# Optimization experiments

Measured on AMD Instinct MI355X. Metric: run time of the kernel, lower is better.

Reference implementation:

```python
import jax, jax.numpy as jnp
import numpy as np

N = 100000      # op nodes
E = 1600000     # feed edges
C = 8           # num_configs
H = 64          # hidden_dim
OPE = 64        # op_embed_dim
NF = 140        # per-node dense features
CF = 18         # per-config features
NUM_OPS = 120
B = 16          # graphs per batch (context segments)
IN_DIM = OPE + NF + CF  # 222
ALPHA = 0.2     # tf.nn.leaky_relu default slope


def setup_inputs() -> dict:
    key = jax.random.key(0)
    ks = jax.random.split(key, 32)

    def w(k, shape, fan_in):
        return jax.random.normal(k, shape, jnp.float32) * (1.0 / np.sqrt(fan_in))

    inp = {
        'node_feats': jax.random.normal(ks[0], (N, NF), jnp.float32),
        'config_feats': jax.random.normal(ks[1], (N, C, CF), jnp.float32),
        'op_ids': jax.random.randint(ks[2], (N,), 0, NUM_OPS, jnp.int32),
        'src': jax.random.randint(ks[3], (E,), 0, N, jnp.int32),
        'dst': jax.random.randint(ks[4], (E,), 0, N, jnp.int32),
        'graph_ids': jnp.sort(jax.random.randint(ks[5], (N,), 0, B, jnp.int32)),
        'op_emb': jax.random.normal(ks[6], (NUM_OPS, OPE), jnp.float32) * 0.05,
        # GNN layer 0 (input dim 222), layers 1,2 (dim 64)
        'W_d0': w(ks[7], (IN_DIM, H), IN_DIM), 'b_d0': jnp.zeros((H,), jnp.float32),
        'W_p0': w(ks[8], (IN_DIM, H), IN_DIM), 'b_p0': jnp.zeros((H,), jnp.float32),
        'W_d1': w(ks[9], (H, H), H), 'b_d1': jnp.zeros((H,), jnp.float32),
        'W_p1': w(ks[10], (H, H), H), 'b_p1': jnp.zeros((H,), jnp.float32),
        'W_d2': w(ks[11], (H, H), H), 'b_d2': jnp.zeros((H,), jnp.float32),
        'W_p2': w(ks[12], (H, H), H), 'b_p2': jnp.zeros((H,), jnp.float32),
        # postnet MLP: Dense(64) -> act -> Dense(64) -> act -> Dense(1)
        'W_m0': w(ks[13], (H, H), H), 'b_m0': jnp.zeros((H,), jnp.float32),
        'W_m1': w(ks[14], (H, H), H), 'b_m1': jnp.zeros((H,), jnp.float32),
        'W_m2': w(ks[15], (H, 1), H), 'b_m2': jnp.zeros((1,), jnp.float32),
    }
    return inp


def _leaky(x):
    return jax.nn.leaky_relu(x, negative_slope=ALPHA)


def _l2norm(x):  # tf.nn.l2_normalize(axis=-1), eps=1e-12
    sq = jnp.sum(x * x, axis=-1, keepdims=True)
    return x * jax.lax.rsqrt(jnp.maximum(sq, 1e-12))


def reference(node_feats, config_feats, op_ids, src, dst, graph_ids, op_emb,
              W_d0, b_d0, W_p0, b_p0, W_d1, b_d1, W_p1, b_p1,
              W_d2, b_d2, W_p2, b_p2, W_m0, b_m0, W_m1, b_m1, W_m2, b_m2):
    # early-join op embedding + node feats (broadcast over configs) + config feats
    base = jnp.concatenate([op_emb[op_ids], node_feats], axis=-1)  # [N, OPE+NF]
    x = jnp.concatenate(
        [jnp.broadcast_to(base[:, None, :], (N, C, OPE + NF)), config_feats],
        axis=-1)  # [N, C, 222]

    def adj_mul(v):  # bidirectional feed adjacency: A + A^T
        return (jax.ops.segment_sum(v[src], dst, num_segments=N)
                + jax.ops.segment_sum(v[dst], src, num_segments=N))

    for (Wd, bd, Wp, bp) in ((W_d0, b_d0, W_p0, b_p0),
                             (W_d1, b_d1, W_p1, b_p1),
                             (W_d2, b_d2, W_p2, b_p2)):
        y = adj_mul(x)                                  # [N, C, D] spmm
        y = _leaky(jnp.einsum('ncd,dh->nch', y, Wd) + bd)
        x = jnp.einsum('ncd,dh->nch', x, Wp) + bp + y   # residual
        x = _l2norm(x)

    pooled = jax.ops.segment_sum(x, graph_ids, num_segments=B)  # [B, C, H]

    h = _leaky(jnp.einsum('bch,hk->bck', pooled, W_m0) + b_m0)
    h = _leaky(jnp.einsum('bch,hk->bck', h, W_m1) + b_m1)
    out = jnp.einsum('bch,hk->bck', h, W_m2) + b_m2     # [B, C, 1]
    return jnp.squeeze(out, -1)                         # [B, C]
```

## Files before the change

### kernel.cpp

```cpp
#include <hip/hip_runtime.h>
#include <hip/hip_bf16.h>

#define NN 100000
#define EE 1600000
#define CC 8
#define HH 64
#define NF 140
#define CF 18
#define BB 16
#define NROWS (NN * CC)
#define ALPHA 0.2f


typedef unsigned short u16;
typedef unsigned int u32;
typedef unsigned char u8;
typedef __attribute__((ext_vector_type(8))) short short8;
typedef __attribute__((ext_vector_type(4))) float f32x4;
typedef __attribute__((ext_vector_type(4))) float fv4;
typedef __attribute__((ext_vector_type(2))) float f32x2;

__device__ __forceinline__ float rdlane(float v, int l) {
    return __int_as_float(__builtin_amdgcn_readlane(__float_as_int(v), l));
}
__device__ __forceinline__ float lrelu(float x) { return x > 0.f ? x : ALPHA * x; }
__device__ __forceinline__ float wave_sum64(float v) {
#pragma unroll
    for (int m = 1; m < 64; m <<= 1) v += __shfl_xor(v, m, 64);
    return v;
}
__device__ __forceinline__ float b2f(u16 u) { return __uint_as_float(((u32)u) << 16); }
__device__ __forceinline__ u32 f2b(float f) {
    u32 u = __float_as_uint(f);
    return (u + 0x7fffu + ((u >> 16) & 1u)) >> 16;
}
__device__ __forceinline__ u32 pack2(float lo, float hi) {
    return f2b(lo) | (f2b(hi) << 16);
}
__device__ __forceinline__ short8 ld_frag(const u16* p) {
    union { uint4 u; short8 s; } c;
    c.u = *(const uint4*)p;
    return c.s;
}

#if __has_builtin(__builtin_amdgcn_cvt_pk_f32_fp8) && __has_builtin(__builtin_amdgcn_cvt_pk_fp8_f32)
#define HAS_HW_FP8 1
#else
#define HAS_HW_FP8 0
#endif

__device__ __forceinline__ float dec8_sw(u32 b) {
    u32 u = ((b & 0x80u) << 24) | ((b & 0x7fu) << 20);
    return __uint_as_float(u) * 0x1.0p+120f;
}
__device__ __forceinline__ u32 enc8_sw(float f) {
    f = fminf(fmaxf(f, -448.f), 448.f);
    u32 u = __float_as_uint(f * 0x1.0p-120f);
    u32 r = u + 0x7ffffu + ((u >> 20) & 1u);
    return ((r >> 24) & 0x80u) | ((r >> 20) & 0x7fu);
}
__device__ __forceinline__ u32 pk4_fp8(float a, float b, float c, float d) {
#if HAS_HW_FP8
    u32 w = 0;
    w = __builtin_amdgcn_cvt_pk_fp8_f32(a, b, w, false);
    w = __builtin_amdgcn_cvt_pk_fp8_f32(c, d, w, true);
    return w;
#else
    return enc8_sw(a) | (enc8_sw(b) << 8) | (enc8_sw(c) << 16) | (enc8_sw(d) << 24);
#endif
}
__device__ __forceinline__ void accf8(float* a, uint2 t) {
#if HAS_HW_FP8
    f32x2 d;
    d = __builtin_amdgcn_cvt_pk_f32_fp8(t.x, false); a[0] += d.x; a[1] += d.y;
    d = __builtin_amdgcn_cvt_pk_f32_fp8(t.x, true);  a[2] += d.x; a[3] += d.y;
    d = __builtin_amdgcn_cvt_pk_f32_fp8(t.y, false); a[4] += d.x; a[5] += d.y;
    d = __builtin_amdgcn_cvt_pk_f32_fp8(t.y, true);  a[6] += d.x; a[7] += d.y;
#else
    u32 w[2] = {t.x, t.y};
#pragma unroll
    for (int q = 0; q < 2; q++) {
        a[q*4+0] += dec8_sw(w[q] & 0xffu);
        a[q*4+1] += dec8_sw((w[q] >> 8) & 0xffu);
        a[q*4+2] += dec8_sw((w[q] >> 16) & 0xffu);
        a[q*4+3] += dec8_sw((w[q] >> 24) & 0xffu);
    }
#endif
}

__global__ __launch_bounds__(256) void deg_count_k(const int* __restrict__ src,
                                                   const int* __restrict__ dst,
                                                   int* __restrict__ deg) {
    int e = blockIdx.x * 256 + threadIdx.x;
    if (e < EE) atomicAdd(&deg[dst[e]], 1);
    else if (e < 2 * EE) atomicAdd(&deg[src[e - EE]], 1);
}

__global__ __launch_bounds__(1024) void scan1_k(const int* __restrict__ deg,
                                                int* __restrict__ row_ptr,
                                                int* __restrict__ bsum, int n) {
    __shared__ int lds[17];
    int i = blockIdx.x * 1024 + threadIdx.x;
    int lane = threadIdx.x & 63, wv = threadIdx.x >> 6;
    int val = (i < n) ? deg[i] : 0;
    int v = val;
#pragma unroll
    for (int d = 1; d < 64; d <<= 1) {
        int t = __shfl_up(v, d, 64);
        if (lane >= d) v += t;
    }
    if (lane == 63) lds[wv] = v;
    __syncthreads();
    if (threadIdx.x == 0) {
        int run = 0;
#pragma unroll
        for (int k = 0; k < 16; k++) { int t = lds[k]; lds[k] = run; run += t; }
        lds[16] = run;
    }
    __syncthreads();
    if (i < n) row_ptr[i] = v - val + lds[wv];
    if (threadIdx.x == 1023) bsum[blockIdx.x] = lds[16];
}

__global__ void scan2_k(int* __restrict__ bsum, int nb) {
    int run = 0;
    for (int b = 0; b < nb; b++) { int t = bsum[b]; bsum[b] = run; run += t; }
    bsum[nb] = run;
}

__global__ __launch_bounds__(1024) void scan3_k(int* __restrict__ row_ptr,
                                                int* __restrict__ cursor,
                                                const int* __restrict__ bsum,
                                                int n, int nb) {
    int i = blockIdx.x * 1024 + threadIdx.x;
    if (i < n) {
        int v = row_ptr[i] + bsum[blockIdx.x];
        row_ptr[i] = v;
        cursor[i] = v;
    }
    if (i == 0) row_ptr[n] = bsum[nb];
}

__global__ __launch_bounds__(256) void place_k(const int* __restrict__ src,
                                               const int* __restrict__ dst,
                                               int* __restrict__ cursor,
                                               int* __restrict__ col,
                                               int c0, int c1) {
    int e = blockIdx.x * 256 + threadIdx.x;
    int node, other;
    if (e < EE) { node = dst[e]; other = src[e]; }
    else if (e < 2 * EE) { node = src[e - EE]; other = dst[e - EE]; }
    else return;
    if (node < c0 || node >= c1) return;
    int pos = atomicAdd(&cursor[node], 1);
    col[pos] = other;
}

__global__ __launch_bounds__(256) void prep_w_k(const float* __restrict__ Wd1, const float* __restrict__ Wp1,
                                                const float* __restrict__ Wd2, const float* __restrict__ Wp2,
                                                const float* __restrict__ Wd0nf, const float* __restrict__ Wp0nf,
                                                u16* __restrict__ WT) {
    int i = blockIdx.x * 256 + threadIdx.x;
    if (i < 4 * 4096) {
        int w = i >> 12, idx = i & 4095;
        int n = idx >> 6, k = idx & 63;
        const float* W = (w == 0) ? Wd1 : (w == 1) ? Wp1 : (w == 2) ? Wd2 : Wp2;
        WT[w * 4096 + n * 64 + k] = (u16)f2b(W[k * 64 + n]);
    } else {
        int j = i - 4 * 4096;
        if (j < 2 * 64 * 160) {
            int w = j / 10240, idx = j % 10240;
            int n = idx / 160, k = idx % 160;
            const float* W = w ? Wp0nf : Wd0nf;
            WT[16384 + w * 10240 + n * 160 + k] = (k < 140) ? (u16)f2b(W[k * 64 + n]) : (u16)0;
        }
    }
}

__global__ __launch_bounds__(256) void op_dp_k(const float* __restrict__ op_emb,
                                               const float* __restrict__ Wd_top,
                                               const float* __restrict__ Wp_top,
                                               float* __restrict__ op_d,
                                               float* __restrict__ op_p) {
    int lane = threadIdx.x & 63;
    int wid = (blockIdx.x * 256 + threadIdx.x) >> 6;
    if (wid >= 120) return;
    float v = op_emb[wid * 64 + lane];
    float ad = 0.f, ap = 0.f;
    for (int k = 0; k < 64; k++) {
        float s = rdlane(v, k);
        ad = fmaf(s, Wd_top[k * 64 + lane], ad);
        ap = fmaf(s, Wp_top[k * 64 + lane], ap);
    }
    op_d[wid * 64 + lane] = ad;
    op_p[wid * 64 + lane] = ap;
}

__global__ __launch_bounds__(256) void nf_mfma_k(const float* __restrict__ nf,
                                                 const u16* __restrict__ WdT0,
                                                 const u16* __restrict__ WpT0,
                                                 u16* __restrict__ nf_d,
                                                 u16* __restrict__ nf_p) {
    int lane = threadIdx.x & 63;
    int m = lane & 15, q = lane >> 4;
    int wid = (blockIdx.x * 256 + threadIdx.x) >> 6;
    int nw = (gridDim.x * 256) >> 6;
    for (int rb = wid; rb < NN / 16; rb += nw) {
        int node0 = rb * 16;
        const float* row = nf + (size_t)(node0 + m) * 140;
        short8 af[5];
#pragma unroll
        for (int s = 0; s < 5; s++) {
            int k0 = s * 32 + q * 8;
            float f[8];
            if (s < 4) {
                fv4 lo = __builtin_nontemporal_load((const fv4*)(row + k0));
                fv4 hi = __builtin_nontemporal_load((const fv4*)(row + k0 + 4));
                f[0]=lo.x; f[1]=lo.y; f[2]=lo.z; f[3]=lo.w;
                f[4]=hi.x; f[5]=hi.y; f[6]=hi.z; f[7]=hi.w;
            } else {
#pragma unroll
                for (int j = 0; j < 8; j++) f[j] = 0.f;
                if (q == 0) {
                    fv4 lo = __builtin_nontemporal_load((const fv4*)(row + 128));
                    fv4 hi = __builtin_nontemporal_load((const fv4*)(row + 132));
                    f[0]=lo.x; f[1]=lo.y; f[2]=lo.z; f[3]=lo.w;
                    f[4]=hi.x; f[5]=hi.y; f[6]=hi.z; f[7]=hi.w;
                } else if (q == 1) {
                    fv4 lo = __builtin_nontemporal_load((const fv4*)(row + 136));
                    f[0]=lo.x; f[1]=lo.y; f[2]=lo.z; f[3]=lo.w;
                }
            }
            short8 t;
#pragma unroll
            for (int j = 0; j < 8; j++) t[j] = (short)f2b(f[j]);
            af[s] = t;
        }
        f32x4 ad[4], ap[4];
#pragma unroll
        for (int t = 0; t < 4; t++) {
            ad[t] = (f32x4){0.f, 0.f, 0.f, 0.f};
            ap[t] = (f32x4){0.f, 0.f, 0.f, 0.f};
        }
#pragma unroll
        for (int s = 0; s < 5; s++) {
#pragma unroll
            for (int t = 0; t < 4; t++) {
                int boff = (t * 16 + m) * 160 + s * 32 + q * 8;
                short8 bdw = ld_frag(WdT0 + boff);
                short8 bpw = ld_frag(WpT0 + boff);
                ad[t] = __builtin_amdgcn_mfma_f32_16x16x32_bf16(af[s], bdw, ad[t], 0, 0, 0);
                ap[t] = __builtin_amdgcn_mfma_f32_16x16x32_bf16(af[s], bpw, ap[t], 0, 0, 0);
            }
        }
#pragma unroll
        for (int r = 0; r < 4; r++) {
            size_t nrow = (size_t)(node0 + q * 4 + r);
#pragma unroll
            for (int t = 0; t < 4; t++) {
                nf_d[nrow * 64 + t * 16 + m] = (u16)f2b(ad[t][r]);
                nf_p[nrow * 64 + t * 16 + m] = (u16)f2b(ap[t][r]);
            }
        }
    }
}

__global__ __launch_bounds__(256) void hd0_dual_k(u8* __restrict__ G,
                                                  u16* __restrict__ Y,
                                                  const float* __restrict__ cf,
                                                  const int* __restrict__ op_ids,
                                                  const u16* __restrict__ nf_d,
                                                  const u16* __restrict__ nf_p,
                                                  const float* __restrict__ op_d,
                                                  const float* __restrict__ op_p,
                                                  const float* __restrict__ WdBot,
                                                  const float* __restrict__ WpBot) {
    int lane = threadIdx.x & 63;
    float wbd[18], wbp[18];
#pragma unroll
    for (int k = 0; k < 18; k++) { wbd[k] = WdBot[k * 64 + lane]; wbp[k] = WpBot[k * 64 + lane]; }
    int wid = (blockIdx.x * 256 + threadIdx.x) >> 6;
    int nw = (gridDim.x * 256) >> 6;
    for (int row = wid; row < NROWS; row += nw) {
        int n = row >> 3;
        float cfv = (lane < 18) ? __builtin_nontemporal_load(cf + (size_t)row * 18 + lane) : 0.f;
        int op = op_ids[n];
        float accd = op_d[op * 64 + lane] + b2f(nf_d[(size_t)n * 64 + lane]);
        float accp = op_p[op * 64 + lane] + b2f(nf_p[(size_t)n * 64 + lane]);
#pragma unroll
        for (int k = 0; k < 18; k++) {
            float s = rdlane(cfv, k);
            accd = fmaf(s, wbd[k], accd);
            accp = fmaf(s, wbp[k], accp);
        }
        float f1 = __shfl_down(accd, 1, 64);
        float f2 = __shfl_down(accd, 2, 64);
        float f3 = __shfl_down(accd, 3, 64);
        if ((lane & 3) == 0)
            ((u32*)G)[(size_t)row * 16 + (lane >> 2)] = pk4_fp8(accd, f1, f2, f3);
        Y[(size_t)row * 64 + lane] = (u16)f2b(accp);
    }
}

__global__ __launch_bounds__(256) void conv_fp8_k(const u16* __restrict__ src,
                                                  uint2* __restrict__ dst) {
    int i = blockIdx.x * 256 + threadIdx.x;
    if (i >= NROWS * 64 / 8) return;
    short8 v = ld_frag(src + (size_t)i * 8);
    float f[8];
#pragma unroll
    for (int k = 0; k < 8; k++) f[k] = b2f((u16)v[k]);
    uint2 o;
    o.x = pk4_fp8(f[0], f[1], f[2], f[3]);
    o.y = pk4_fp8(f[4], f[5], f[6], f[7]);
    dst[i] = o;
}

__global__ __launch_bounds__(256) void fused_l0_f8_k(const u8* __restrict__ G,
                                                     u16* __restrict__ Y,
                                                     const int* __restrict__ row_ptr,
                                                     const int* __restrict__ col,
                                                     const float* __restrict__ bd,
                                                     const float* __restrict__ bp) {
    int wid = (blockIdx.x * 256 + threadIdx.x) >> 6;
    int lane = threadIdx.x & 63;
    if (wid >= NN) return;
    int r = lane >> 3, fb = (lane & 7) * 8;
    const uint2* G2 = (const uint2*)G;
    int start = row_ptr[wid];
    int end = row_ptr[wid + 1];
    float a[8] = {0.f, 0.f, 0.f, 0.f, 0.f, 0.f, 0.f, 0.f};
    int j = start;
    for (; j + 16 <= end; j += 16) {
        uint2 t[16];
#pragma unroll
        for (int u = 0; u < 16; u++) t[u] = G2[(size_t)col[j + u] * 64 + lane];
#pragma unroll
        for (int u = 0; u < 16; u++) accf8(a, t[u]);
    }
    for (; j + 4 <= end; j += 4) {
        uint2 t[4];
#pragma unroll
        for (int u = 0; u < 4; u++) t[u] = G2[(size_t)col[j + u] * 64 + lane];
#pragma unroll
        for (int u = 0; u < 4; u++) accf8(a, t[u]);
    }
    for (; j < end; j++) {
        uint2 t0 = G2[(size_t)col[j] * 64 + lane];
        accf8(a, t0);
    }
    float bdv[8], bpv[8];
#pragma unroll
    for (int jj = 0; jj < 8; jj++) { bdv[jj] = bd[fb + jj]; bpv[jj] = bp[fb + jj]; }
    size_t rowg = (size_t)wid * 8 + r;
    short8 xp = ld_frag(Y + rowg * 64 + fb);
    float v[8], sq = 0.f;
#pragma unroll
    for (int q = 0; q < 8; q++) {
        float val = b2f((u16)xp[q]) + bpv[q] + lrelu(a[q] + bdv[q]);
        v[q] = val;
        sq += val * val;
    }
    sq += __shfl_xor(sq, 1, 64);
    sq += __shfl_xor(sq, 2, 64);
    sq += __shfl_xor(sq, 4, 64);
    float sc = rsqrtf(fmaxf(sq, 1e-12f));
    uint4 o;
    o.x = pack2(v[0] * sc, v[1] * sc);
    o.y = pack2(v[2] * sc, v[3] * sc);
    o.z = pack2(v[4] * sc, v[5] * sc);
    o.w = pack2(v[6] * sc, v[7] * sc);
    *(uint4*)(Y + rowg * 64 + fb) = o;
}

__global__ __launch_bounds__(256) void fused_spmm_f8_k(u16* __restrict__ Y,
                                                       const u8* __restrict__ G,
                                                       const int* __restrict__ row_ptr,
                                                       const int* __restrict__ col,
                                                       const u16* __restrict__ WdT,
                                                       const u16* __restrict__ WpT,
                                                       const float* __restrict__ bd,
                                                       const float* __restrict__ bp) {
    __shared__ u16 lds_t[4 * 16 * 72];
    int lane = threadIdx.x & 63;
    u16* L = lds_t + (threadIdx.x >> 6) * (16 * 72);
    int m = lane & 15, q = lane >> 4;
    const uint2* G2 = (const uint2*)G;

    int wid = (blockIdx.x * 256 + threadIdx.x) >> 6;
    if (wid >= NN / 2) return;
    int pb = wid;

#pragma unroll
    for (int p = 0; p < 2; p++) {
        int node = pb * 2 + p;
        int start = row_ptr[node], end = row_ptr[node + 1];
        float a[8] = {0.f, 0.f, 0.f, 0.f, 0.f, 0.f, 0.f, 0.f};
        int j = start;
        for (; j + 16 <= end; j += 16) {
            uint2 t[16];
#pragma unroll
            for (int u = 0; u < 16; u++) t[u] = G2[(size_t)col[j + u] * 64 + lane];
#pragma unroll
            for (int u = 0; u < 16; u++) accf8(a, t[u]);
        }
        for (; j + 4 <= end; j += 4) {
            uint2 t[4];
#pragma unroll
            for (int u = 0; u < 4; u++) t[u] = G2[(size_t)col[j + u] * 64 + lane];
#pragma unroll
            for (int u = 0; u < 4; u++) accf8(a, t[u]);
        }
        for (; j < end; j++) {
            uint2 t0 = G2[(size_t)col[j] * 64 + lane];
            accf8(a, t0);
        }
        uint4 o;
        o.x = pack2(a[0], a[1]);
        o.y = pack2(a[2], a[3]);
        o.z = pack2(a[4], a[5]);
        o.w = pack2(a[6], a[7]);
        *(uint4*)(L + (size_t)(p * 8 + (lane >> 3)) * 72 + (lane & 7) * 8) = o;
    }
    __builtin_amdgcn_sched_barrier(0);

    short8 ay0 = ld_frag(L + m * 72 + q * 8);
    short8 ay1 = ld_frag(L + m * 72 + 32 + q * 8);
    const u16* xr = Y + ((size_t)(pb * 16 + m)) * 64 + q * 8;
    short8 ax0 = ld_frag(xr), ax1 = ld_frag(xr + 32);
    float v[4][4], sq[4];
#pragma unroll
    for (int r = 0; r < 4; r++) sq[r] = 0.f;
#pragma unroll 1
    for (int t = 0; t < 4; t++) {
        int off = (t * 16 + m) * 64 + q * 8;
        short8 bd0 = ld_frag(WdT + off), bd1 = ld_frag(WdT + off + 32);
        short8 bp0 = ld_frag(WpT + off), bp1 = ld_frag(WpT + off + 32);
        f32x4 ad = (f32x4){0.f, 0.f, 0.f, 0.f};
        f32x4 ap = (f32x4){0.f, 0.f, 0.f, 0.f};
        ad = __builtin_amdgcn_mfma_f32_16x16x32_bf16(ay0, bd0, ad, 0, 0, 0);
        ad = __builtin_amdgcn_mfma_f32_16x16x32_bf16(ay1, bd1, ad, 0, 0, 0);
        ap = __builtin_amdgcn_mfma_f32_16x16x32_bf16(ax0, bp0, ap, 0, 0, 0);
        ap = __builtin_amdgcn_mfma_f32_16x16x32_bf16(ax1, bp1, ap, 0, 0, 0);
        float bdv = bd[t * 16 + m], bpv = bp[t * 16 + m];
#pragma unroll
        for (int r = 0; r < 4; r++) {
            float val = ap[r] + bpv + lrelu(ad[r] + bdv);
            v[t][r] = val;
            sq[r] += val * val;
        }
    }
#pragma unroll
    for (int r = 0; r < 4; r++) {
#pragma unroll
        for (int mm = 1; mm < 16; mm <<= 1) sq[r] += __shfl_xor(sq[r], mm, 64);
        float sc = rsqrtf(fmaxf(sq[r], 1e-12f));
        u16* orow = Y + ((size_t)(pb * 16 + q * 4 + r)) * 64 + m;
#pragma unroll
        for (int t = 0; t < 4; t++) orow[t * 16] = (u16)f2b(v[t][r] * sc);
    }
}

__global__ __launch_bounds__(256) void pool2_k(const u16* __restrict__ X,
                                               const int* __restrict__ graph_ids,
                                               float* __restrict__ pooled) {
    int chunk = (NN + gridDim.x - 1) / gridDim.x;
    int n0 = blockIdx.x * chunk;
    int n1 = min(n0 + chunk, NN);
    if (n0 >= n1) return;
    int f = threadIdx.x & 63;
    int c0 = threadIdx.x >> 6;
    float a0 = 0.f, a1 = 0.f;
    int cur = graph_ids[n0];
    for (int n = n0; n < n1; n++) {
        int g = graph_ids[n];
        if (g != cur) {
            atomicAdd(&pooled[(size_t)(cur * 8 + c0) * 64 + f], a0);
            atomicAdd(&pooled[(size_t)(cur * 8 + c0 + 4) * 64 + f], a1);
            a0 = 0.f; a1 = 0.f; cur = g;
        }
        a0 += b2f(X[((size_t)n * 8 + c0) * 64 + f]);
        a1 += b2f(X[((size_t)n * 8 + c0 + 4) * 64 + f]);
    }
    atomicAdd(&pooled[(size_t)(cur * 8 + c0) * 64 + f], a0);
    atomicAdd(&pooled[(size_t)(cur * 8 + c0 + 4) * 64 + f], a1);
}

__global__ __launch_bounds__(256) void mlp_k(const float* __restrict__ pooled,
                                             const float* __restrict__ W0, const float* __restrict__ b0,
                                             const float* __restrict__ W1, const float* __restrict__ b1,
                                             const float* __restrict__ W2, const float* __restrict__ b2,
                                             float* __restrict__ out) {
    int lane = threadIdx.x & 63;
    int row = blockIdx.x * 4 + (threadIdx.x >> 6);
    if (row >= BB * CC) return;
    float b0l = b0[lane], b1l = b1[lane], w2l = W2[lane], b2s = b2[0];
    float p = pooled[(size_t)row * 64 + lane];
    float a = 0.f;
    for (int k = 0; k < 64; k++) a = fmaf(rdlane(p, k), W0[k * 64 + lane], a);
    float h0 = lrelu(a + b0l);
    float a1 = 0.f;
    for (int k = 0; k < 64; k++) a1 = fmaf(rdlane(h0, k), W1[k * 64 + lane], a1);
    float h1 = lrelu(a1 + b1l);
    float v = wave_sum64(h1 * w2l);
    if (lane == 0) out[row] = v + b2s;
}

extern "C" void kernel_launch(void* const* d_in, const int* in_sizes, int n_in,
                              void* d_out, int out_size, void* d_ws, size_t ws_size,
                              hipStream_t stream) {
    const float* node_feats   = (const float*)d_in[0];
    const float* config_feats = (const float*)d_in[1];
    const int*   op_ids       = (const int*)d_in[2];
    const int*   src          = (const int*)d_in[3];
    const int*   dst          = (const int*)d_in[4];
    const int*   graph_ids    = (const int*)d_in[5];
    const float* op_emb       = (const float*)d_in[6];
    const float* W_d0 = (const float*)d_in[7],  *b_d0 = (const float*)d_in[8];
    const float* W_p0 = (const float*)d_in[9],  *b_p0 = (const float*)d_in[10];
    const float* W_d1 = (const float*)d_in[11], *b_d1 = (const float*)d_in[12];
    const float* W_p1 = (const float*)d_in[13], *b_p1 = (const float*)d_in[14];
    const float* W_d2 = (const float*)d_in[15], *b_d2 = (const float*)d_in[16];
    const float* W_p2 = (const float*)d_in[17], *b_p2 = (const float*)d_in[18];
    const float* W_m0 = (const float*)d_in[19], *b_m0 = (const float*)d_in[20];
    const float* W_m1 = (const float*)d_in[21], *b_m1 = (const float*)d_in[22];
    const float* W_m2 = (const float*)d_in[23], *b_m2 = (const float*)d_in[24];
    float* out = (float*)d_out;

    char* ws = (char*)d_ws;
    size_t off = 0;
    u16* Y       = (u16*)(ws + off); off += (size_t)NROWS * 64 * 2;
    u8*  G       = (u8*)(ws + off);  off += (size_t)NROWS * 64;
    int* col     = (int*)(ws + off);   off += (size_t)2 * EE * 4;
    int* row_ptr = (int*)(ws + off);   off += 400128;
    u16* WT      = (u16*)(ws + off);   off += (4 * 4096 + 2 * 10240) * 2;
    float* pooled = (float*)(ws + off); off += BB * CC * 64 * 4;
    u16* nf_d    = (u16*)(ws + off); off += (size_t)NN * 64 * 2;
    u16* nf_p    = (u16*)(ws + off); off += (size_t)NN * 64 * 2;
    float* op_d  = (float*)(ws + off); off += 120 * 64 * 4;
    float* op_p  = (float*)(ws + off); off += 120 * 64 * 4;
    int* deg     = (int*)(ws + off);   off += 400128;
    int* cursor  = (int*)(ws + off);   off += 400128;
    int* bsum    = (int*)(ws + off);   off += 512;
    (void)ws_size; (void)in_sizes; (void)n_in; (void)out_size;

    const int NB = (NN + 1023) / 1024;
    const int NCONV = (NROWS * 64 / 8 + 255) / 256;

    hipMemsetAsync(deg, 0, (size_t)NN * 4, stream);
    hipMemsetAsync(pooled, 0, (size_t)BB * CC * 64 * 4, stream);
    deg_count_k<<<(2 * EE) / 256, 256, 0, stream>>>(src, dst, deg);
    prep_w_k<<<144, 256, 0, stream>>>(W_d1, W_p1, W_d2, W_p2,
                                      W_d0 + 64 * 64, W_p0 + 64 * 64, WT);
    scan1_k<<<NB, 1024, 0, stream>>>(deg, row_ptr, bsum, NN);
    scan2_k<<<1, 1, 0, stream>>>(bsum, NB);
    scan3_k<<<NB, 1024, 0, stream>>>(row_ptr, cursor, bsum, NN, NB);
    {
        const int NCHUNK = 8;
        const int CSZ = (NN + NCHUNK - 1) / NCHUNK;
        for (int c = 0; c < NCHUNK; c++) {
            int c0 = c * CSZ;
            int c1 = min(c0 + CSZ, NN);
            place_k<<<(2 * EE) / 256, 256, 0, stream>>>(src, dst, cursor, col, c0, c1);
        }
    }

    op_dp_k<<<30, 256, 0, stream>>>(op_emb, W_d0, W_p0, op_d, op_p);
    nf_mfma_k<<<512, 256, 0, stream>>>(node_feats, WT + 16384, WT + 16384 + 10240, nf_d, nf_p);
    hd0_dual_k<<<2048, 256, 0, stream>>>(G, Y, config_feats, op_ids, nf_d, nf_p,
                                         op_d, op_p, W_d0 + 204 * 64, W_p0 + 204 * 64);

    fused_l0_f8_k<<<NN / 4, 256, 0, stream>>>(G, Y, row_ptr, col, b_d0, b_p0);
    conv_fp8_k<<<NCONV, 256, 0, stream>>>(Y, (uint2*)G);
    fused_spmm_f8_k<<<12500, 256, 0, stream>>>(Y, G, row_ptr, col,
                                               WT, WT + 4096, b_d1, b_p1);
    conv_fp8_k<<<NCONV, 256, 0, stream>>>(Y, (uint2*)G);
    fused_spmm_f8_k<<<12500, 256, 0, stream>>>(Y, G, row_ptr, col,
                                               WT + 8192, WT + 12288, b_d2, b_p2);

    pool2_k<<<2048, 256, 0, stream>>>(Y, graph_ids, pooled);
    mlp_k<<<32, 256, 0, stream>>>(pooled, W_m0, b_m0, W_m1, b_m1, W_m2, b_m2, out);
}
```

Before: 1.536 ms.

## Merge setup kernels, parallelize block-sum scan, widen fp8 conversion, halve placement passes

Merges the degree count, weight prep and op-embedding projection into one launch that dispatches on block index. The serial single-thread block-sum scan becomes a 128-thread wave scan. The fp8 conversion kernel now handles 16 values per thread with 128-bit stores. Edge placement runs in 4 chunked passes instead of 8, which cuts launches but may add atomic contention per pass. Together these aim to reduce launch count and small serial overheads in the graph-setup phase.

```diff
diff --git a/kernel.cpp b/kernel.cpp
--- a/kernel.cpp
+++ b/kernel.cpp
@@ -88,12 +88,62 @@
 #endif
 }
 
-__global__ __launch_bounds__(256) void deg_count_k(const int* __restrict__ src,
-                                                   const int* __restrict__ dst,
-                                                   int* __restrict__ deg) {
-    int e = blockIdx.x * 256 + threadIdx.x;
-    if (e < EE) atomicAdd(&deg[dst[e]], 1);
-    else if (e < 2 * EE) atomicAdd(&deg[src[e - EE]], 1);
+#define SETUP_DEG_BLK 12500
+#define SETUP_PW_BLK  144
+#define SETUP_OP_BLK  30
+__global__ __launch_bounds__(256) void setup_k(const int* __restrict__ src,
+                                               const int* __restrict__ dst,
+                                               int* __restrict__ deg,
+                                               const float* __restrict__ Wd1, const float* __restrict__ Wp1,
+                                               const float* __restrict__ Wd2, const float* __restrict__ Wp2,
+                                               const float* __restrict__ Wd0nf, const float* __restrict__ Wp0nf,
+                                               u16* __restrict__ WT,
+                                               const float* __restrict__ op_emb,
+                                               const float* __restrict__ Wd_top,
+                                               const float* __restrict__ Wp_top,
+                                               float* __restrict__ op_d,
+                                               float* __restrict__ op_p) {
+    int b = blockIdx.x;
+    if (b < SETUP_DEG_BLK) {
+        int e = b * 256 + threadIdx.x;
+        if (e < EE) atomicAdd(&deg[dst[e]], 1);
+        else if (e < 2 * EE) atomicAdd(&deg[src[e - EE]], 1);
+        return;
+    }
+    b -= SETUP_DEG_BLK;
+    if (b < SETUP_PW_BLK) {
+        int i = b * 256 + threadIdx.x;
+        if (i < 4 * 4096) {
+            int w = i >> 12, idx = i & 4095;
+            int n = idx >> 6, k = idx & 63;
+            const float* W = (w == 0) ? Wd1 : (w == 1) ? Wp1 : (w == 2) ? Wd2 : Wp2;
+            WT[w * 4096 + n * 64 + k] = (u16)f2b(W[k * 64 + n]);
+        } else {
+            int j = i - 4 * 4096;
+            if (j < 2 * 64 * 160) {
+                int w = j / 10240, idx = j % 10240;
+                int n = idx / 160, k = idx % 160;
+                const float* W = w ? Wp0nf : Wd0nf;
+                WT[16384 + w * 10240 + n * 160 + k] = (k < 140) ? (u16)f2b(W[k * 64 + n]) : (u16)0;
+            }
+        }
+        return;
+    }
+    b -= SETUP_PW_BLK;
+    {
+        int lane = threadIdx.x & 63;
+        int wid = (b * 256 + threadIdx.x) >> 6;
+        if (wid >= 120) return;
+        float v = op_emb[wid * 64 + lane];
+        float ad = 0.f, ap = 0.f;
+        for (int k = 0; k < 64; k++) {
+            float s = rdlane(v, k);
+            ad = fmaf(s, Wd_top[k * 64 + lane], ad);
+            ap = fmaf(s, Wp_top[k * 64 + lane], ap);
+        }
+        op_d[wid * 64 + lane] = ad;
+        op_p[wid * 64 + lane] = ap;
+    }
 }
 
 __global__ __launch_bounds__(1024) void scan1_k(const int* __restrict__ deg,
@@ -122,10 +172,22 @@
     if (threadIdx.x == 1023) bsum[blockIdx.x] = lds[16];
 }
 
-__global__ void scan2_k(int* __restrict__ bsum, int nb) {
-    int run = 0;
-    for (int b = 0; b < nb; b++) { int t = bsum[b]; bsum[b] = run; run += t; }
-    bsum[nb] = run;
+__global__ __launch_bounds__(128) void scan2_k(int* __restrict__ bsum, int nb) {
+    __shared__ int wsum[2];
+    int tid = threadIdx.x;
+    int lane = tid & 63, wv = tid >> 6;
+    int val = (tid < nb) ? bsum[tid] : 0;
+    int v = val;
+#pragma unroll
+    for (int d = 1; d < 64; d <<= 1) {
+        int t = __shfl_up(v, d, 64);
+        if (lane >= d) v += t;
+    }
+    if (lane == 63) wsum[wv] = v;
+    __syncthreads();
+    int incl = v + ((wv == 1) ? wsum[0] : 0);
+    if (tid < nb) bsum[tid] = incl - val;
+    if (tid == 127) bsum[nb] = incl;
 }
 
 __global__ __launch_bounds__(1024) void scan3_k(int* __restrict__ row_ptr,
@@ -156,46 +218,6 @@
     col[pos] = other;
 }
 
-__global__ __launch_bounds__(256) void prep_w_k(const float* __restrict__ Wd1, const float* __restrict__ Wp1,
-                                                const float* __restrict__ Wd2, const float* __restrict__ Wp2,
-                                                const float* __restrict__ Wd0nf, const float* __restrict__ Wp0nf,
-                                                u16* __restrict__ WT) {
-    int i = blockIdx.x * 256 + threadIdx.x;
-    if (i < 4 * 4096) {
-        int w = i >> 12, idx = i & 4095;
-        int n = idx >> 6, k = idx & 63;
-        const float* W = (w == 0) ? Wd1 : (w == 1) ? Wp1 : (w == 2) ? Wd2 : Wp2;
-        WT[w * 4096 + n * 64 + k] = (u16)f2b(W[k * 64 + n]);
-    } else {
-        int j = i - 4 * 4096;
-        if (j < 2 * 64 * 160) {
-            int w = j / 10240, idx = j % 10240;
-            int n = idx / 160, k = idx % 160;
-            const float* W = w ? Wp0nf : Wd0nf;
-            WT[16384 + w * 10240 + n * 160 + k] = (k < 140) ? (u16)f2b(W[k * 64 + n]) : (u16)0;
-        }
-    }
-}
-
-__global__ __launch_bounds__(256) void op_dp_k(const float* __restrict__ op_emb,
-                                               const float* __restrict__ Wd_top,
-                                               const float* __restrict__ Wp_top,
-                                               float* __restrict__ op_d,
-                                               float* __restrict__ op_p) {
-    int lane = threadIdx.x & 63;
-    int wid = (blockIdx.x * 256 + threadIdx.x) >> 6;
-    if (wid >= 120) return;
-    float v = op_emb[wid * 64 + lane];
-    float ad = 0.f, ap = 0.f;
-    for (int k = 0; k < 64; k++) {
-        float s = rdlane(v, k);
-        ad = fmaf(s, Wd_top[k * 64 + lane], ad);
-        ap = fmaf(s, Wp_top[k * 64 + lane], ap);
-    }
-    op_d[wid * 64 + lane] = ad;
-    op_p[wid * 64 + lane] = ap;
-}
-
 __global__ __launch_bounds__(256) void nf_mfma_k(const float* __restrict__ nf,
                                                  const u16* __restrict__ WdT0,
                                                  const u16* __restrict__ WpT0,
@@ -303,16 +325,19 @@
 }
 
 __global__ __launch_bounds__(256) void conv_fp8_k(const u16* __restrict__ src,
-                                                  uint2* __restrict__ dst) {
+                                                  uint4* __restrict__ dst) {
     int i = blockIdx.x * 256 + threadIdx.x;
-    if (i >= NROWS * 64 / 8) return;
-    short8 v = ld_frag(src + (size_t)i * 8);
-    float f[8];
-#pragma unroll
-    for (int k = 0; k < 8; k++) f[k] = b2f((u16)v[k]);
-    uint2 o;
+    if (i >= NROWS * 4) return;
+    short8 v0 = ld_frag(src + (size_t)i * 16);
+    short8 v1 = ld_frag(src + (size_t)i * 16 + 8);
+    float f[16];
+#pragma unroll
+    for (int k = 0; k < 8; k++) { f[k] = b2f((u16)v0[k]); f[k + 8] = b2f((u16)v1[k]); }
+    uint4 o;
     o.x = pk4_fp8(f[0], f[1], f[2], f[3]);
     o.y = pk4_fp8(f[4], f[5], f[6], f[7]);
+    o.z = pk4_fp8(f[8], f[9], f[10], f[11]);
+    o.w = pk4_fp8(f[12], f[13], f[14], f[15]);
     dst[i] = o;
 }
 
@@ -545,18 +570,19 @@
     (void)ws_size; (void)in_sizes; (void)n_in; (void)out_size;
 
     const int NB = (NN + 1023) / 1024;
-    const int NCONV = (NROWS * 64 / 8 + 255) / 256;
+    const int NCONV = NROWS * 4 / 256;
 
     hipMemsetAsync(deg, 0, (size_t)NN * 4, stream);
     hipMemsetAsync(pooled, 0, (size_t)BB * CC * 64 * 4, stream);
-    deg_count_k<<<(2 * EE) / 256, 256, 0, stream>>>(src, dst, deg);
-    prep_w_k<<<144, 256, 0, stream>>>(W_d1, W_p1, W_d2, W_p2,
-                                      W_d0 + 64 * 64, W_p0 + 64 * 64, WT);
+    setup_k<<<SETUP_DEG_BLK + SETUP_PW_BLK + SETUP_OP_BLK, 256, 0, stream>>>(
+        src, dst, deg,
+        W_d1, W_p1, W_d2, W_p2, W_d0 + 64 * 64, W_p0 + 64 * 64, WT,
+        op_emb, W_d0, W_p0, op_d, op_p);
     scan1_k<<<NB, 1024, 0, stream>>>(deg, row_ptr, bsum, NN);
-    scan2_k<<<1, 1, 0, stream>>>(bsum, NB);
+    scan2_k<<<1, 128, 0, stream>>>(bsum, NB);
     scan3_k<<<NB, 1024, 0, stream>>>(row_ptr, cursor, bsum, NN, NB);
     {
-        const int NCHUNK = 8;
+        const int NCHUNK = 4;
         const int CSZ = (NN + NCHUNK - 1) / NCHUNK;
         for (int c = 0; c < NCHUNK; c++) {
             int c0 = c * CSZ;
@@ -565,16 +591,15 @@
         }
     }
 
-    op_dp_k<<<30, 256, 0, stream>>>(op_emb, W_d0, W_p0, op_d, op_p);
     nf_mfma_k<<<512, 256, 0, stream>>>(node_feats, WT + 16384, WT + 16384 + 10240, nf_d, nf_p);
     hd0_dual_k<<<2048, 256, 0, stream>>>(G, Y, config_feats, op_ids, nf_d, nf_p,
                                          op_d, op_p, W_d0 + 204 * 64, W_p0 + 204 * 64);
 
     fused_l0_f8_k<<<NN / 4, 256, 0, stream>>>(G, Y, row_ptr, col, b_d0, b_p0);
-    conv_fp8_k<<<NCONV, 256, 0, stream>>>(Y, (uint2*)G);
+    conv_fp8_k<<<NCONV, 256, 0, stream>>>(Y, (uint4*)G);
     fused_spmm_f8_k<<<12500, 256, 0, stream>>>(Y, G, row_ptr, col,
                                                WT, WT + 4096, b_d1, b_p1);
-    conv_fp8_k<<<NCONV, 256, 0, stream>>>(Y, (uint2*)G);
+    conv_fp8_k<<<NCONV, 256, 0, stream>>>(Y, (uint4*)G);
     fused_spmm_f8_k<<<12500, 256, 0, stream>>>(Y, G, row_ptr, col,
                                                WT + 8192, WT + 12288, b_d2, b_p2);
 
```

Result: no change. 1.520 ms (-1.0%).
